# Performance work log

Hardware: AMD Instinct MI355X
Metric: run time of the kernel (lower is better)

The kernel has to match this reference:

```python
import jax, jax.numpy as jnp
import numpy as np

COST_CLASS = 1.0


def _lsa(cost):
    """linear_sum_assignment clone (Jonker-Volgenant shortest augmenting path),
    matching scipy.optimize.linear_sum_assignment semantics for rectangular inputs."""
    cost = np.asarray(cost, dtype=np.float64)
    transposed = cost.shape[0] > cost.shape[1]
    if transposed:
        cost = cost.T
    nr, nc = cost.shape
    u = np.zeros(nr)
    v = np.zeros(nc)
    path = np.full(nc, -1, dtype=np.int64)
    col4row = np.full(nr, -1, dtype=np.int64)
    row4col = np.full(nc, -1, dtype=np.int64)
    for cur in range(nr):
        i = cur
        SR = np.zeros(nr, dtype=bool)
        SC = np.zeros(nc, dtype=bool)
        d = np.full(nc, np.inf)
        minVal = 0.0
        sink = -1
        while sink == -1:
            SR[i] = True
            rem = ~SC
            r = minVal + cost[i, rem] - u[i] - v[rem]
            dr = d[rem]
            pr = path[rem]
            better = r < dr
            dr[better] = r[better]
            pr[better] = i
            d[rem] = dr
            path[rem] = pr
            remIdx = np.flatnonzero(rem)
            j = remIdx[np.argmin(d[remIdx])]
            minVal = d[j]
            SC[j] = True
            if row4col[j] == -1:
                sink = j
            else:
                i = row4col[j]
        # dual updates (scipy _lsap_body)
        u[cur] += minVal
        mask = SR.copy()
        mask[cur] = False
        u[mask] += minVal - d[col4row[mask]]
        v[SC] -= minVal - d[SC]
        # augment along shortest path
        j = sink
        while True:
            i = path[j]
            row4col[j] = i
            col4row[i], j = j, col4row[i]
            if i == cur:
                break
    if transposed:
        order = np.argsort(col4row)
        return col4row[order], order
    return np.arange(nr), col4row


def setup_inputs() -> dict:
    key = jax.random.key(0)
    k1, k2, k3 = jax.random.split(key, 3)
    bs, Q, T, NC = 32, 256, 128, 2048
    pred_logits = jax.random.normal(k1, (bs, Q, NC), dtype=jnp.float32)
    tgt_labels = jax.random.randint(k2, (bs, T), 0, NC)
    agent_mask = jax.random.randint(k3, (bs, Q), 0, 2).astype(bool)
    return {"pred_logits": pred_logits, "tgt_labels": tgt_labels,
            "agent_mask": agent_mask, "use_background": 0}


def reference(pred_logits, tgt_labels, agent_mask, use_background):
    bs, Q, _ = pred_logits.shape
    T = tgt_labels.shape[1]
    probs = jax.nn.softmax(pred_logits, axis=-1)  # [bs, Q, NC]
    if not use_background:
        probs = jnp.where(agent_mask[:, :, None], probs, 0.0)
    out_prob = probs.reshape(bs * Q, -1)
    tgt_ids = tgt_labels.reshape(-1)                  # concat of all batch labels
    C = COST_CLASS * (-out_prob[:, tgt_ids])          # [bs*Q, bs*T]
    C = C.reshape(bs, Q, bs * T)
    # per-batch Hungarian (same as scipy loop in the original; inherently serial per instance)
    Cn = np.asarray(C)
    rows = np.empty((bs, T), dtype=np.int64)
    cols = np.empty((bs, T), dtype=np.int64)
    for i in range(bs):
        r, c = _lsa(Cn[i, :, i * T:(i + 1) * T])      # [Q, T] block for batch i
        rows[i] = r
        cols[i] = c
    return C, jnp.asarray(rows), jnp.asarray(cols)
```

## Files before the change

### kernel.cpp

```cpp
#include <hip/hip_runtime.h>
#include <hip/hip_bf16.h>
#include <math.h>

#define BS 32
#define QN 256
#define TN 128
#define NCLS 2048
#define NTGT (BS * TN)

__global__ void detect_mask_layout(const unsigned char* __restrict__ m, int* flag) {
    __shared__ int found;
    if (threadIdx.x == 0) found = 0;
    __syncthreads();
    int local = 0;
    for (int i = threadIdx.x; i < BS * QN; i += blockDim.x) {
        if ((i & 3) != 0 && m[i] != 0) local = 1;
    }
    if (local) atomicOr(&found, 1);
    __syncthreads();
    if (threadIdx.x == 0) *flag = found;
}

__global__ __launch_bounds__(256) void compute_C_kernel(
    const float* __restrict__ logits, const int* __restrict__ labels,
    const unsigned char* __restrict__ mask_b, const int* __restrict__ use_bg,
    const int* __restrict__ layout_flag, float* __restrict__ C,
    float* __restrict__ CT) {
    __shared__ float prob_sh[NCLS];
    __shared__ float red[4];

    const int tid = threadIdx.x;
    const int bq = blockIdx.x;
    const float* row = logits + (size_t)bq * NCLS;

    const float4 xa = ((const float4*)row)[tid];
    const float4 xb = ((const float4*)row)[tid + 256];

    float m = fmaxf(fmaxf(fmaxf(xa.x, xa.y), fmaxf(xa.z, xa.w)),
                    fmaxf(fmaxf(xb.x, xb.y), fmaxf(xb.z, xb.w)));
#pragma unroll
    for (int off = 32; off >= 1; off >>= 1) m = fmaxf(m, __shfl_xor(m, off));
    if ((tid & 63) == 0) red[tid >> 6] = m;
    __syncthreads();
    m = fmaxf(fmaxf(red[0], red[1]), fmaxf(red[2], red[3]));
    __syncthreads();

    float4 ea, eb;
    ea.x = expf(xa.x - m);
    ea.y = expf(xa.y - m);
    ea.z = expf(xa.z - m);
    ea.w = expf(xa.w - m);
    eb.x = expf(xb.x - m);
    eb.y = expf(xb.y - m);
    eb.z = expf(xb.z - m);
    eb.w = expf(xb.w - m);
    float s = ((ea.x + ea.y) + (ea.z + ea.w)) + ((eb.x + eb.y) + (eb.z + eb.w));
#pragma unroll
    for (int off = 32; off >= 1; off >>= 1) s += __shfl_xor(s, off);
    if ((tid & 63) == 0) red[tid >> 6] = s;
    __syncthreads();
    s = ((red[0] + red[1]) + red[2]) + red[3];

    ((float4*)prob_sh)[tid] = make_float4(ea.x / s, ea.y / s, ea.z / s, ea.w / s);
    ((float4*)prob_sh)[tid + 256] = make_float4(eb.x / s, eb.y / s, eb.z / s, eb.w / s);

    const int ub = *use_bg;
    int am;
    if (*layout_flag)
        am = mask_b[bq];
    else
        am = ((const int*)mask_b)[bq];
    const bool zero_row = (ub == 0) && (am == 0);
    __syncthreads();

    float* Crow = C + (size_t)bq * NTGT;
    const int4* lab4 = (const int4*)labels;
    if (zero_row) {
        const float4 z = make_float4(0.f, 0.f, 0.f, 0.f);
#pragma unroll
        for (int k = 0; k < 4; k++) ((float4*)Crow)[tid + k * 256] = z;
    } else {
#pragma unroll
        for (int k = 0; k < 4; k++) {
            const int4 l = lab4[tid + k * 256];
            float4 o;
            o.x = -prob_sh[l.x];
            o.y = -prob_sh[l.y];
            o.z = -prob_sh[l.z];
            o.w = -prob_sh[l.w];
            ((float4*)Crow)[tid + k * 256] = o;
        }
    }

    if (CT != nullptr && tid < TN) {
        const int bb = bq >> 8;
        const int q = bq & 255;
        const int lab = labels[bb * TN + tid];
        CT[(size_t)bb * TN * QN + (size_t)tid * QN + q] =
            zero_row ? 0.0f : -prob_sh[lab];
    }
}

template <int CTRL>
__device__ __forceinline__ double dpp_mov_f64(double x) {
    union { double d; int i[2]; } a, r;
    a.d = x;
    r.i[0] = __builtin_amdgcn_update_dpp(0, a.i[0], CTRL, 0xF, 0xF, true);
    r.i[1] = __builtin_amdgcn_update_dpp(0, a.i[1], CTRL, 0xF, 0xF, true);
    return r.d;
}
__device__ __forceinline__ double read_lane_f64(double x, int srclane) {
    union { double d; int i[2]; } a, r;
    a.d = x;
    r.i[0] = __builtin_amdgcn_readlane(a.i[0], srclane);
    r.i[1] = __builtin_amdgcn_readlane(a.i[1], srclane);
    return r.d;
}

#define QUAD_XOR1 0xB1
#define QUAD_XOR2 0x4E
#define ROW_ROR4  0x124
#define ROW_ROR8  0x128

__global__ __launch_bounds__(64) void lsa_kernel(const float* __restrict__ C,
                                                 const float* __restrict__ CT,
                                                 float* __restrict__ rows_out,
                                                 float* __restrict__ cols_out) {
    const int b = blockIdx.x;
    const int lane = threadIdx.x;
    const int j0 = lane * 4;

    __shared__ float cost_sh[TN * QN];
    __shared__ double u_sh[TN];
    __shared__ int path_sh[QN];
    __shared__ int row4col_sh[QN];
    __shared__ int col4row_sh[TN];

    u_sh[lane] = 0.0;
    u_sh[lane + 64] = 0.0;
    col4row_sh[lane] = -1;
    col4row_sh[lane + 64] = -1;
#pragma unroll
    for (int t = 0; t < 4; t++) row4col_sh[lane + 64 * t] = -1;

    double v0 = 0.0, v1 = 0.0, v2 = 0.0, v3 = 0.0;
    double u0 = 0.0, u1 = 0.0;

    if (CT) {
        const float4* src = (const float4*)(CT + (size_t)b * TN * QN);
        float4* dst = (float4*)cost_sh;
#pragma unroll 8
        for (int it = 0; it < TN * QN / 4 / 64; it++) {
            const int idx = it * 64 + lane;
            dst[idx] = src[idx];
        }
    } else {
        const float* cbsrc = C + (size_t)b * QN * NTGT + b * TN;
        for (int it = 0; it < 512; it++) {
            const int j = it >> 1;
            const int i = lane + 64 * (it & 1);
            cost_sh[i * QN + j] = cbsrc[(size_t)j * NTGT + i];
        }
    }
    __syncthreads();

    for (int cur = 0; cur < TN; cur++) {
        double dv0 = INFINITY, dv1 = INFINITY, dv2 = INFINITY, dv3 = INFINITY;
        double dm0 = INFINITY, dm1 = INFINITY, dm2 = INFINITY, dm3 = INFINITY;
        double du0 = 0.0, du1 = 0.0;
        int sc = 0, sr = 0;
        int p0 = 0, p1 = 0, p2 = 0, p3 = 0;
        const int4 rcv = *(const int4*)&row4col_sh[j0];
        if (lane == (cur >> 1)) sr = 1 << (cur & 1);

        int i = cur;
        double m_d = 0.0;
        bool need_reduce = true;
        unsigned long long B0 = 0, B1 = 0, B2 = 0, B3 = 0;
        int sink;

        while (true) {
            const float4 cc = *(const float4*)(cost_sh + i * QN + j0);
            const double ui = u_sh[i];

            const double ca0 = ((m_d + (double)cc.x) - ui) - v0;
            const double ca1 = ((m_d + (double)cc.y) - ui) - v1;
            const double ca2 = ((m_d + (double)cc.z) - ui) - v2;
            const double ca3 = ((m_d + (double)cc.w) - ui) - v3;
            const bool i0 = !(sc & 1) && (ca0 < dv0);
            const bool i1 = !(sc & 2) && (ca1 < dv1);
            const bool i2 = !(sc & 4) && (ca2 < dv2);
            const bool i3 = !(sc & 8) && (ca3 < dv3);
            const unsigned long long anyI =
                __ballot(i0) | __ballot(i1) | __ballot(i2) | __ballot(i3);
            if (i0) { dv0 = ca0; dm0 = ca0; p0 = i; }
            if (i1) { dv1 = ca1; dm1 = ca1; p1 = i; }
            if (i2) { dv2 = ca2; dm2 = ca2; p2 = i; }
            if (i3) { dv3 = ca3; dm3 = ca3; p3 = i; }

            if (anyI != 0ull || need_reduce) {
                double lm = fmin(fmin(dm0, dm1), fmin(dm2, dm3));
                lm = fmin(lm, dpp_mov_f64<QUAD_XOR1>(lm));
                lm = fmin(lm, dpp_mov_f64<QUAD_XOR2>(lm));
                lm = fmin(lm, dpp_mov_f64<ROW_ROR4>(lm));
                lm = fmin(lm, dpp_mov_f64<ROW_ROR8>(lm));
                const double r0 = read_lane_f64(lm, 0);
                const double r1 = read_lane_f64(lm, 16);
                const double r2 = read_lane_f64(lm, 32);
                const double r3 = read_lane_f64(lm, 48);
                m_d = fmin(fmin(r0, r1), fmin(r2, r3));
                B0 = __ballot(dm0 == m_d);
                B1 = __ballot(dm1 == m_d);
                B2 = __ballot(dm2 == m_d);
                B3 = __ballot(dm3 == m_d);
            }

            int jmin = 0x7fffffff;
            if (B0) { const int c = ((__ffsll((long long)B0) - 1) << 2) + 0; jmin = c < jmin ? c : jmin; }
            if (B1) { const int c = ((__ffsll((long long)B1) - 1) << 2) + 1; jmin = c < jmin ? c : jmin; }
            if (B2) { const int c = ((__ffsll((long long)B2) - 1) << 2) + 2; jmin = c < jmin ? c : jmin; }
            if (B3) { const int c = ((__ffsll((long long)B3) - 1) << 2) + 3; jmin = c < jmin ? c : jmin; }
            const int owner = jmin >> 2;
            const int slot = jmin & 3;
            const unsigned long long bit = 1ull << owner;
            if (slot == 0) B0 &= ~bit;
            else if (slot == 1) B1 &= ~bit;
            else if (slot == 2) B2 &= ~bit;
            else B3 &= ~bit;

            if (lane == owner) {
                sc |= 1 << slot;
                if (slot == 0) dm0 = INFINITY;
                else if (slot == 1) dm1 = INFINITY;
                else if (slot == 2) dm2 = INFINITY;
                else dm3 = INFINITY;
            }

            const int sa = (slot & 1) ? rcv.y : rcv.x;
            const int sb = (slot & 1) ? rcv.w : rcv.z;
            const int rcsel = (slot & 2) ? sb : sa;
            const int krc = __builtin_amdgcn_readlane(rcsel, owner);
            if (krc < 0) { sink = jmin; break; }

            if (lane == (krc >> 1)) {
                if (krc & 1) { du1 = m_d; sr |= 2; }
                else { du0 = m_d; sr |= 1; }
            }
            i = krc;
            need_reduce = ((B0 | B1 | B2 | B3) == 0ull);
        }

        path_sh[lane] = p0;
        path_sh[lane + 64] = p1;
        path_sh[lane + 128] = p2;
        path_sh[lane + 192] = p3;
        if (sc & 1) v0 -= m_d - dv0;
        if (sc & 2) v1 -= m_d - dv1;
        if (sc & 4) v2 -= m_d - dv2;
        if (sc & 8) v3 -= m_d - dv3;
        if (sr & 1) u0 += (2 * lane == cur) ? m_d : (m_d - du0);
        if (sr & 2) u1 += (2 * lane + 1 == cur) ? m_d : (m_d - du1);
        u_sh[2 * lane] = u0;
        u_sh[2 * lane + 1] = u1;
        __syncthreads();

        if (lane == 0) {
            int j = sink;
            while (true) {
                const int pi = path_sh[(j & 3) * 64 + (j >> 2)];
                row4col_sh[j] = pi;
                const int nj = col4row_sh[pi];
                col4row_sh[pi] = j;
                j = nj;
                if (pi == cur) break;
            }
        }
        __syncthreads();
    }

#pragma unroll
    for (int t = 0; t < 2; t++) {
        const int ii = lane + 64 * t;
        const int myv = col4row_sh[ii];
        int rank = 0;
        for (int t2 = 0; t2 < TN; t2++) rank += (col4row_sh[t2] < myv) ? 1 : 0;
        rows_out[b * TN + rank] = (float)myv;
        cols_out[b * TN + rank] = (float)ii;
    }
}

extern "C" void kernel_launch(void* const* d_in, const int* in_sizes, int n_in,
                              void* d_out, int out_size, void* d_ws, size_t ws_size,
                              hipStream_t stream) {
    const float* logits = (const float*)d_in[0];
    const int* labels = (const int*)d_in[1];
    const unsigned char* mask_b = (const unsigned char*)d_in[2];
    const int* use_bg = (const int*)d_in[3];

    float* C = (float*)d_out;
    float* rows_out = C + (size_t)BS * QN * NTGT;
    float* cols_out = rows_out + BS * TN;

    int* flag = (int*)d_ws;
    const size_t ct_off = 4096;
    const size_t ct_bytes = (size_t)BS * TN * QN * sizeof(float);
    const bool useCT = ws_size >= ct_off + ct_bytes;
    float* CT = useCT ? (float*)((char*)d_ws + ct_off) : nullptr;

    detect_mask_layout<<<1, 256, 0, stream>>>(mask_b, flag);
    compute_C_kernel<<<BS * QN, 256, 0, stream>>>(logits, labels, mask_b, use_bg, flag, C, CT);
    lsa_kernel<<<BS, 64, 0, stream>>>(C, CT, rows_out, cols_out);
}
```

Before: 1.151 ms.

## Overlap Hungarian solve with full cost-matrix write in a fused kernel

Splits the work into a small kernel that only produces the transposed per-batch cost blocks (CT), followed by one fused launch. In that launch the first 32 blocks run the serial LSA solver from CT while the remaining blocks recompute softmax and write the large C output, so the big memory-bound write can overlap the latency-bound assignment solve. The trade-offs are that softmax is computed twice, so logits are read twice. The C-writing blocks also run as single 64-thread waves and carry the solver's roughly 128KB LDS allocation, which limits their occupancy to about one block per CU.

```diff
diff --git a/kernel.cpp b/kernel.cpp
--- a/kernel.cpp
+++ b/kernel.cpp
@@ -21,11 +21,10 @@
     if (threadIdx.x == 0) *flag = found;
 }
 
-__global__ __launch_bounds__(256) void compute_C_kernel(
+__global__ __launch_bounds__(256) void ct_kernel(
     const float* __restrict__ logits, const int* __restrict__ labels,
     const unsigned char* __restrict__ mask_b, const int* __restrict__ use_bg,
-    const int* __restrict__ layout_flag, float* __restrict__ C,
-    float* __restrict__ CT) {
+    const int* __restrict__ layout_flag, float* __restrict__ CT) {
     __shared__ float prob_sh[NCLS];
     __shared__ float red[4];
 
@@ -73,6 +72,66 @@
     const bool zero_row = (ub == 0) && (am == 0);
     __syncthreads();
 
+    if (tid < TN) {
+        const int bb = bq >> 8;
+        const int q = bq & 255;
+        const int lab = labels[bb * TN + tid];
+        CT[(size_t)bb * TN * QN + (size_t)tid * QN + q] =
+            zero_row ? 0.0f : -prob_sh[lab];
+    }
+}
+
+__global__ __launch_bounds__(256) void compute_C_kernel(
+    const float* __restrict__ logits, const int* __restrict__ labels,
+    const unsigned char* __restrict__ mask_b, const int* __restrict__ use_bg,
+    const int* __restrict__ layout_flag, float* __restrict__ C) {
+    __shared__ float prob_sh[NCLS];
+    __shared__ float red[4];
+
+    const int tid = threadIdx.x;
+    const int bq = blockIdx.x;
+    const float* row = logits + (size_t)bq * NCLS;
+
+    const float4 xa = ((const float4*)row)[tid];
+    const float4 xb = ((const float4*)row)[tid + 256];
+
+    float m = fmaxf(fmaxf(fmaxf(xa.x, xa.y), fmaxf(xa.z, xa.w)),
+                    fmaxf(fmaxf(xb.x, xb.y), fmaxf(xb.z, xb.w)));
+#pragma unroll
+    for (int off = 32; off >= 1; off >>= 1) m = fmaxf(m, __shfl_xor(m, off));
+    if ((tid & 63) == 0) red[tid >> 6] = m;
+    __syncthreads();
+    m = fmaxf(fmaxf(red[0], red[1]), fmaxf(red[2], red[3]));
+    __syncthreads();
+
+    float4 ea, eb;
+    ea.x = expf(xa.x - m);
+    ea.y = expf(xa.y - m);
+    ea.z = expf(xa.z - m);
+    ea.w = expf(xa.w - m);
+    eb.x = expf(xb.x - m);
+    eb.y = expf(xb.y - m);
+    eb.z = expf(xb.z - m);
+    eb.w = expf(xb.w - m);
+    float s = ((ea.x + ea.y) + (ea.z + ea.w)) + ((eb.x + eb.y) + (eb.z + eb.w));
+#pragma unroll
+    for (int off = 32; off >= 1; off >>= 1) s += __shfl_xor(s, off);
+    if ((tid & 63) == 0) red[tid >> 6] = s;
+    __syncthreads();
+    s = ((red[0] + red[1]) + red[2]) + red[3];
+
+    ((float4*)prob_sh)[tid] = make_float4(ea.x / s, ea.y / s, ea.z / s, ea.w / s);
+    ((float4*)prob_sh)[tid + 256] = make_float4(eb.x / s, eb.y / s, eb.z / s, eb.w / s);
+
+    const int ub = *use_bg;
+    int am;
+    if (*layout_flag)
+        am = mask_b[bq];
+    else
+        am = ((const int*)mask_b)[bq];
+    const bool zero_row = (ub == 0) && (am == 0);
+    __syncthreads();
+
     float* Crow = C + (size_t)bq * NTGT;
     const int4* lab4 = (const int4*)labels;
     if (zero_row) {
@@ -91,14 +150,6 @@
             ((float4*)Crow)[tid + k * 256] = o;
         }
     }
-
-    if (CT != nullptr && tid < TN) {
-        const int bb = bq >> 8;
-        const int q = bq & 255;
-        const int lab = labels[bb * TN + tid];
-        CT[(size_t)bb * TN * QN + (size_t)tid * QN + q] =
-            zero_row ? 0.0f : -prob_sh[lab];
-    }
 }
 
 template <int CTRL>
@@ -122,19 +173,12 @@
 #define ROW_ROR4  0x124
 #define ROW_ROR8  0x128
 
-__global__ __launch_bounds__(64) void lsa_kernel(const float* __restrict__ C,
-                                                 const float* __restrict__ CT,
-                                                 float* __restrict__ rows_out,
-                                                 float* __restrict__ cols_out) {
-    const int b = blockIdx.x;
-    const int lane = threadIdx.x;
+__device__ __forceinline__ void lsa_solve(
+    const float* __restrict__ C, const float* __restrict__ CT,
+    float* __restrict__ rows_out, float* __restrict__ cols_out,
+    int b, int lane,
+    float* cost_sh, double* u_sh, int* path_sh, int* row4col_sh, int* col4row_sh) {
     const int j0 = lane * 4;
-
-    __shared__ float cost_sh[TN * QN];
-    __shared__ double u_sh[TN];
-    __shared__ int path_sh[QN];
-    __shared__ int row4col_sh[QN];
-    __shared__ int col4row_sh[TN];
 
     u_sh[lane] = 0.0;
     u_sh[lane + 64] = 0.0;
@@ -289,6 +333,97 @@
     }
 }
 
+__global__ __launch_bounds__(64) void lsa_kernel(const float* __restrict__ C,
+                                                 const float* __restrict__ CT,
+                                                 float* __restrict__ rows_out,
+                                                 float* __restrict__ cols_out) {
+    __shared__ float cost_sh[TN * QN];
+    __shared__ double u_sh[TN];
+    __shared__ int path_sh[QN];
+    __shared__ int row4col_sh[QN];
+    __shared__ int col4row_sh[TN];
+    lsa_solve(C, CT, rows_out, cols_out, blockIdx.x, threadIdx.x,
+              cost_sh, u_sh, path_sh, row4col_sh, col4row_sh);
+}
+
+__global__ __launch_bounds__(64) void fused_kernel(
+    const float* __restrict__ logits, const int* __restrict__ labels,
+    const unsigned char* __restrict__ mask_b, const int* __restrict__ use_bg,
+    const int* __restrict__ layout_flag, const float* __restrict__ CT,
+    float* __restrict__ C, float* __restrict__ rows_out,
+    float* __restrict__ cols_out) {
+    __shared__ float cost_sh[TN * QN];
+    __shared__ double u_sh[TN];
+    __shared__ int path_sh[QN];
+    __shared__ int row4col_sh[QN];
+    __shared__ int col4row_sh[TN];
+
+    const int lane = threadIdx.x;
+
+    if (blockIdx.x >= BS) {
+        const int bq = blockIdx.x - BS;
+        const float* row = logits + (size_t)bq * NCLS;
+
+        float4 x[8];
+#pragma unroll
+        for (int k = 0; k < 8; k++) x[k] = ((const float4*)row)[lane + 64 * k];
+
+        float m = -INFINITY;
+#pragma unroll
+        for (int k = 0; k < 8; k++)
+            m = fmaxf(m, fmaxf(fmaxf(x[k].x, x[k].y), fmaxf(x[k].z, x[k].w)));
+#pragma unroll
+        for (int off = 32; off >= 1; off >>= 1) m = fmaxf(m, __shfl_xor(m, off));
+
+        float s = 0.f;
+        float4 e[8];
+#pragma unroll
+        for (int k = 0; k < 8; k++) {
+            e[k].x = expf(x[k].x - m);
+            e[k].y = expf(x[k].y - m);
+            e[k].z = expf(x[k].z - m);
+            e[k].w = expf(x[k].w - m);
+            s += ((e[k].x + e[k].y) + (e[k].z + e[k].w));
+        }
+#pragma unroll
+        for (int off = 32; off >= 1; off >>= 1) s += __shfl_xor(s, off);
+
+        float* prob = cost_sh;
+#pragma unroll
+        for (int k = 0; k < 8; k++)
+            ((float4*)prob)[lane + 64 * k] =
+                make_float4(e[k].x / s, e[k].y / s, e[k].z / s, e[k].w / s);
+
+        const int ub = *use_bg;
+        int am;
+        if (*layout_flag)
+            am = mask_b[bq];
+        else
+            am = ((const int*)mask_b)[bq];
+        const bool zero_row = (ub == 0) && (am == 0);
+        __syncthreads();
+
+        float* Crow = C + (size_t)bq * NTGT;
+        const int4* lab4 = (const int4*)labels;
+        if (zero_row) {
+            const float4 z = make_float4(0.f, 0.f, 0.f, 0.f);
+#pragma unroll
+            for (int k = 0; k < 16; k++) ((float4*)Crow)[lane + 64 * k] = z;
+        } else {
+#pragma unroll
+            for (int k = 0; k < 16; k++) {
+                const int4 l = lab4[lane + 64 * k];
+                ((float4*)Crow)[lane + 64 * k] =
+                    make_float4(-prob[l.x], -prob[l.y], -prob[l.z], -prob[l.w]);
+            }
+        }
+        return;
+    }
+
+    lsa_solve(nullptr, CT, rows_out, cols_out, blockIdx.x, lane,
+              cost_sh, u_sh, path_sh, row4col_sh, col4row_sh);
+}
+
 extern "C" void kernel_launch(void* const* d_in, const int* in_sizes, int n_in,
                               void* d_out, int out_size, void* d_ws, size_t ws_size,
                               hipStream_t stream) {
@@ -308,6 +443,13 @@
     float* CT = useCT ? (float*)((char*)d_ws + ct_off) : nullptr;
 
     detect_mask_layout<<<1, 256, 0, stream>>>(mask_b, flag);
-    compute_C_kernel<<<BS * QN, 256, 0, stream>>>(logits, labels, mask_b, use_bg, flag, C, CT);
-    lsa_kernel<<<BS, 64, 0, stream>>>(C, CT, rows_out, cols_out);
-}
+    if (useCT) {
+        ct_kernel<<<BS * QN, 256, 0, stream>>>(logits, labels, mask_b, use_bg, flag, CT);
+        fused_kernel<<<BS + BS * QN, 64, 0, stream>>>(logits, labels, mask_b, use_bg,
+                                                      flag, CT, C, rows_out, cols_out);
+    } else {
+        compute_C_kernel<<<BS * QN, 256, 0, stream>>>(logits, labels, mask_b, use_bg,
+                                                      flag, C);
+        lsa_kernel<<<BS, 64, 0, stream>>>(C, nullptr, rows_out, cols_out);
+    }
+}
```

Measured after the change: 1.129 ms. About the same (-1.9%).
